# Kernel tuning notes

Hardware: AMD Instinct MI355X
Metric: run time of the kernel (lower is better)

## Reference

```python
import jax, jax.numpy as jnp
import numpy as np

N_NODES = 100000
N_EDGES = 1000000
D = 64
N_LAYERS = 3
N_GRAPHS = 64


def _sage_layer(x, src, dst, W_l, b_l, W_r, n_nodes):
    # PyG SAGEConv (aggr='mean'): out = lin_l(mean_{j in N(i)} x_j) + lin_r(x_i)
    msgs = x[src]  # [E, d] gather
    agg = jax.ops.segment_sum(msgs, dst, num_segments=n_nodes)  # [N, d]
    deg = jax.ops.segment_sum(jnp.ones((src.shape[0],), x.dtype), dst, num_segments=n_nodes)
    agg = agg / jnp.maximum(deg, 1.0)[:, None]
    return agg @ W_l + b_l + x @ W_r


def setup_inputs() -> dict:
    key = jax.random.key(0)
    k = jax.random.split(key, 6)
    scale = 1.0 / np.sqrt(D)
    x = jax.random.normal(k[0], (N_NODES, D), dtype=jnp.float32)
    edge_index = jax.random.randint(k[1], (2, N_EDGES), 0, N_NODES, dtype=jnp.int64)
    batch = jnp.sort(jax.random.randint(k[2], (N_NODES,), 0, N_GRAPHS, dtype=jnp.int64))
    Wl = jax.random.normal(k[3], (N_LAYERS, D, D), dtype=jnp.float32) * scale
    bl = jax.random.normal(k[4], (N_LAYERS, D), dtype=jnp.float32) * scale
    Wr = jax.random.normal(k[5], (N_LAYERS, D, D), dtype=jnp.float32) * scale
    return {"x": x, "edge_index": edge_index, "batch": batch,
            "Wl": Wl, "bl": bl, "Wr": Wr, "num_graphs": N_GRAPHS}


def reference(x, edge_index, batch, Wl, bl, Wr, num_graphs):
    src, dst = edge_index[0], edge_index[1]
    n_nodes = x.shape[0]
    for l in range(Wl.shape[0]):  # small fixed number of layers
        x = _sage_layer(x, src, dst, Wl[l], bl[l], Wr[l], n_nodes)
    # per-graph masked mean pooling == segment mean over batch ids
    sums = jax.ops.segment_sum(x, batch, num_segments=num_graphs)  # [G, d]
    counts = jax.ops.segment_sum(jnp.ones((n_nodes,), x.dtype), batch, num_segments=num_graphs)
    return sums / jnp.maximum(counts, 1.0)[:, None]
```

## Files before the change

### kernel.cpp

```cpp
#include <hip/hip_runtime.h>


#define DD 64
#define NBA 128
#define CAP 4096

typedef __attribute__((ext_vector_type(8))) short short8;
typedef __attribute__((ext_vector_type(4))) float f32x4;

__device__ inline short8 pack4(unsigned a, unsigned b, unsigned c, unsigned d) {
    union { uint4 u; short8 s; } un;
    un.u = make_uint4(a, b, c, d);
    return un.s;
}

__device__ inline short8 as_short8(uint4 u) {
    union { uint4 u4; short8 s; } un;
    un.u4 = u;
    return un.s;
}

__device__ inline unsigned rne_bf16(float v) {
    unsigned u = __float_as_uint(v);
    return (u + 0x7FFFu + ((u >> 16) & 1u)) >> 16;
}

__global__ __launch_bounds__(256) void bucket_count(
    const int* __restrict__ dst, int* __restrict__ cnt, int E, int NBUCK) {
    extern __shared__ int hist[];
    const int b = blockIdx.x;
    const int per = (E + NBA - 1) / NBA;
    const int lo = b * per, hi = min(lo + per, E);
    for (int k = threadIdx.x; k < NBUCK; k += 256) hist[k] = 0;
    __syncthreads();
    for (int e = lo + threadIdx.x; e < hi; e += 256)
        atomicAdd(&hist[dst[e] >> 8], 1);
    __syncthreads();
    for (int k = threadIdx.x; k < NBUCK; k += 256)
        cnt[b * NBUCK + k] = hist[k];
}

__global__ __launch_bounds__(256) void bucket_prescan(
    const int* __restrict__ cnt, int* __restrict__ base,
    int* __restrict__ tot, int NBUCK) {
    const int lane = threadIdx.x & 63;
    const int k = (int)((blockIdx.x * 256 + threadIdx.x) >> 6);
    if (k >= NBUCK) return;
    int v0 = cnt[(size_t)lane * NBUCK + k];
    int v1 = cnt[(size_t)(lane + 64) * NBUCK + k];
    int s0 = v0, s1 = v1;
#pragma unroll
    for (int o = 1; o < 64; o <<= 1) {
        const int u0 = __shfl_up(s0, o, 64);
        const int u1 = __shfl_up(s1, o, 64);
        if (lane >= o) { s0 += u0; s1 += u1; }
    }
    const int total0 = __shfl(s0, 63, 64);
    base[(size_t)lane * NBUCK + k] = s0 - v0;
    base[(size_t)(lane + 64) * NBUCK + k] = total0 + s1 - v1;
    if (lane == 63) tot[k] = total0 + s1;
}

__global__ __launch_bounds__(1024) void bucket_toff(
    const int* __restrict__ tot, int* __restrict__ boff,
    int* __restrict__ offs, int NBUCK, int E, int N) {
    __shared__ int s[1024];
    __shared__ int carry_s;
    const int t = threadIdx.x;
    if (t == 0) carry_s = 0;
    __syncthreads();
    for (int cs = 0; cs < NBUCK; cs += 1024) {
        const int i = cs + t;
        const int v = (i < NBUCK) ? tot[i] : 0;
        s[t] = v;
        __syncthreads();
        for (int o = 1; o < 1024; o <<= 1) {
            const int a = (t >= o) ? s[t - o] : 0;
            __syncthreads();
            s[t] += a;
            __syncthreads();
        }
        const int carry = carry_s;
        if (i < NBUCK) boff[i] = carry + s[t] - v;
        __syncthreads();
        if (t == 1023) carry_s = carry + s[1023];
        __syncthreads();
    }
    if (t == 0) { boff[NBUCK] = E; offs[N] = E; }
}

__global__ __launch_bounds__(256) void bucket_scatter(
    const int* __restrict__ src, const int* __restrict__ dst,
    const int* __restrict__ base, const int* __restrict__ boff,
    unsigned* __restrict__ ebuf, int E, int NBUCK) {
    extern __shared__ int pos[];
    const int b = blockIdx.x;
    const int per = (E + NBA - 1) / NBA;
    const int lo = b * per, hi = min(lo + per, E);
    for (int k = threadIdx.x; k < NBUCK; k += 256)
        pos[k] = base[b * NBUCK + k] + boff[k];
    __syncthreads();
    for (int e = lo + threadIdx.x; e < hi; e += 256) {
        const int d = dst[e];
        const int s = src[e];
        const int p = atomicAdd(&pos[d >> 8], 1);
        ebuf[p] = ((unsigned)(d & 255) << 24) | (unsigned)s;
    }
}

__global__ __launch_bounds__(256) void bucket_sort(
    const unsigned* __restrict__ ebuf, const int* __restrict__ boff,
    int* __restrict__ offs, int* __restrict__ adj, int N) {
    const int b  = blockIdx.x;
    const int lo = boff[b];
    const int sz = boff[b + 1] - lo;
    const int base = b << 8;
    const int t = threadIdx.x;

    __shared__ int hist[256];
    __shared__ int hcur[256];
    __shared__ unsigned sbuf[CAP];

    hist[t] = 0;
    __syncthreads();
    for (int i = t; i < sz; i += 256)
        atomicAdd(&hist[ebuf[lo + i] >> 24], 1);
    __syncthreads();
    int v = hist[t];
    hcur[t] = v;
    __syncthreads();
    for (int o = 1; o < 256; o <<= 1) {
        const int a = (t >= o) ? hcur[t - o] : 0;
        __syncthreads();
        hcur[t] += a;
        __syncthreads();
    }
    const int ex = hcur[t] - v;
    __syncthreads();
    hcur[t] = ex;
    if (base + t < N) offs[base + t] = lo + ex;
    __syncthreads();

    if (sz <= CAP) {
        for (int i = t; i < sz; i += 256) {
            const unsigned w = ebuf[lo + i];
            const int p = atomicAdd(&hcur[w >> 24], 1);
            sbuf[p] = w & 0x00FFFFFFu;
        }
        __syncthreads();
        for (int i = t; i < sz; i += 256) adj[lo + i] = (int)sbuf[i];
    } else {
        for (int i = t; i < sz; i += 256) {
            const unsigned w = ebuf[lo + i];
            const int p = atomicAdd(&hcur[w >> 24], 1);
            adj[lo + p] = (int)(w & 0x00FFFFFFu);
        }
    }
}

__global__ __launch_bounds__(256) void cast_bf16(
    const float* __restrict__ in, unsigned short* __restrict__ outb, long long n8) {
    const long long t = (long long)blockIdx.x * 256 + threadIdx.x;
    if (t >= n8) return;
    const float4 v0 = *reinterpret_cast<const float4*>(in + t * 8);
    const float4 v1 = *reinterpret_cast<const float4*>(in + t * 8 + 4);
    uint4 o;
    o.x = rne_bf16(v0.x) | (rne_bf16(v0.y) << 16);
    o.y = rne_bf16(v0.z) | (rne_bf16(v0.w) << 16);
    o.z = rne_bf16(v1.x) | (rne_bf16(v1.y) << 16);
    o.w = rne_bf16(v1.z) | (rne_bf16(v1.w) << 16);
    *reinterpret_cast<uint4*>(outb + t * 8) = o;
}

__global__ __launch_bounds__(256) void aggregate_bf16(
    const unsigned short* __restrict__ xb, unsigned short* __restrict__ aggb,
    const int* __restrict__ offs, const int* __restrict__ adj, int n) {
    const int t  = blockIdx.x * 256 + threadIdx.x;
    const int nd = t >> 3;
    const int c8 = (t & 7) * 8;
    if (nd >= n) return;

    const int s = offs[nd];
    const int e = offs[nd + 1];

    float a0[8], a1[8], a2[8], a3[8];
#pragma unroll
    for (int p = 0; p < 8; ++p) { a0[p] = 0.f; a1[p] = 0.f; a2[p] = 0.f; a3[p] = 0.f; }

#define ACC8(A, U)                                                             \
    do {                                                                       \
        A[0] += __uint_as_float((U).x << 16);                                  \
        A[1] += __uint_as_float((U).x & 0xFFFF0000u);                          \
        A[2] += __uint_as_float((U).y << 16);                                  \
        A[3] += __uint_as_float((U).y & 0xFFFF0000u);                          \
        A[4] += __uint_as_float((U).z << 16);                                  \
        A[5] += __uint_as_float((U).z & 0xFFFF0000u);                          \
        A[6] += __uint_as_float((U).w << 16);                                  \
        A[7] += __uint_as_float((U).w & 0xFFFF0000u);                          \
    } while (0)

    int j = s;
    for (; j + 8 <= e; j += 8) {
        const int i0 = adj[j],     i1 = adj[j + 1], i2 = adj[j + 2], i3 = adj[j + 3];
        const int i4 = adj[j + 4], i5 = adj[j + 5], i6 = adj[j + 6], i7 = adj[j + 7];
        const uint4 u0 = *reinterpret_cast<const uint4*>(xb + (size_t)i0 * DD + c8);
        const uint4 u1 = *reinterpret_cast<const uint4*>(xb + (size_t)i1 * DD + c8);
        const uint4 u2 = *reinterpret_cast<const uint4*>(xb + (size_t)i2 * DD + c8);
        const uint4 u3 = *reinterpret_cast<const uint4*>(xb + (size_t)i3 * DD + c8);
        const uint4 u4 = *reinterpret_cast<const uint4*>(xb + (size_t)i4 * DD + c8);
        const uint4 u5 = *reinterpret_cast<const uint4*>(xb + (size_t)i5 * DD + c8);
        const uint4 u6 = *reinterpret_cast<const uint4*>(xb + (size_t)i6 * DD + c8);
        const uint4 u7 = *reinterpret_cast<const uint4*>(xb + (size_t)i7 * DD + c8);
        ACC8(a0, u0); ACC8(a1, u1); ACC8(a2, u2); ACC8(a3, u3);
        ACC8(a0, u4); ACC8(a1, u5); ACC8(a2, u6); ACC8(a3, u7);
    }
    for (; j + 4 <= e; j += 4) {
        const int i0 = adj[j], i1 = adj[j + 1], i2 = adj[j + 2], i3 = adj[j + 3];
        const uint4 u0 = *reinterpret_cast<const uint4*>(xb + (size_t)i0 * DD + c8);
        const uint4 u1 = *reinterpret_cast<const uint4*>(xb + (size_t)i1 * DD + c8);
        const uint4 u2 = *reinterpret_cast<const uint4*>(xb + (size_t)i2 * DD + c8);
        const uint4 u3 = *reinterpret_cast<const uint4*>(xb + (size_t)i3 * DD + c8);
        ACC8(a0, u0); ACC8(a1, u1); ACC8(a2, u2); ACC8(a3, u3);
    }
    for (; j < e; ++j) {
        const uint4 u = *reinterpret_cast<const uint4*>(xb + (size_t)adj[j] * DD + c8);
        ACC8(a0, u);
    }
#undef ACC8

    const int deg = e - s;
    const float inv = (deg > 0) ? (1.0f / (float)deg) : 1.0f;
    float r[8];
#pragma unroll
    for (int p = 0; p < 8; ++p) r[p] = (a0[p] + a1[p] + a2[p] + a3[p]) * inv;
    uint4 o;
    o.x = rne_bf16(r[0]) | (rne_bf16(r[1]) << 16);
    o.y = rne_bf16(r[2]) | (rne_bf16(r[3]) << 16);
    o.z = rne_bf16(r[4]) | (rne_bf16(r[5]) << 16);
    o.w = rne_bf16(r[6]) | (rne_bf16(r[7]) << 16);
    *reinterpret_cast<uint4*>(aggb + (size_t)nd * DD + c8) = o;
}

__global__ void pack_B(const float* __restrict__ Wl, const float* __restrict__ Wr,
                       unsigned* __restrict__ Bp, int L) {
    int t = blockIdx.x * 256 + threadIdx.x;
    int wv = t >> 6, lane = t & 63;
    if (wv >= L * 16) return;
    int layer = wv >> 4;
    int fid = wv & 15;
    int ks = fid >> 2, nt = fid & 3;
    int j = nt * 16 + (lane & 15);
    int kb = ks * 32 + (lane >> 4) * 8;
    const float* wl = Wl + (size_t)layer * DD * DD;
    const float* wr = Wr + (size_t)layer * DD * DD;
    unsigned hi[8], lo[8];
#pragma unroll
    for (int s = 0; s < 8; ++s) {
        int k = kb + s;
        float v = (k < DD) ? wl[k * DD + j] : wr[(k - DD) * DD + j];
        unsigned u = __float_as_uint(v);
        unsigned h = u & 0xFFFF0000u;
        hi[s] = h;
        float lf = v - __uint_as_float(h);
        lo[s] = __float_as_uint(lf) & 0xFFFF0000u;
    }
    size_t base_hi = ((size_t)(layer * 2 + 0) * 16 + fid) * 64 + lane;
    size_t base_lo = ((size_t)(layer * 2 + 1) * 16 + fid) * 64 + lane;
#pragma unroll
    for (int p = 0; p < 4; ++p) {
        Bp[base_hi * 4 + p] = (hi[2 * p] >> 16) | hi[2 * p + 1];
        Bp[base_lo * 4 + p] = (lo[2 * p] >> 16) | lo[2 * p + 1];
    }
}

__global__ __launch_bounds__(256, 2) void mfma_gemm(
    const unsigned short* __restrict__ gb, const unsigned short* __restrict__ xb,
    unsigned short* __restrict__ outb, const unsigned* __restrict__ Bp,
    const float* __restrict__ bias, int n) {
    const int lane = threadIdx.x & 63;
    const int wv   = (int)((blockIdx.x * 256 + threadIdx.x) >> 6);
    const int nwv  = (int)((gridDim.x * 256) >> 6);

    short8 Bh[4][4], Bl[4][4];
#pragma unroll
    for (int ks = 0; ks < 4; ++ks)
#pragma unroll
        for (int nt = 0; nt < 4; ++nt) {
            int fid = ks * 4 + nt;
            const uint4 h = *reinterpret_cast<const uint4*>(Bp + ((size_t)fid * 64 + lane) * 4);
            const uint4 l = *reinterpret_cast<const uint4*>(Bp + ((size_t)(16 + fid) * 64 + lane) * 4);
            Bh[ks][nt] = pack4(h.x, h.y, h.z, h.w);
            Bl[ks][nt] = pack4(l.x, l.y, l.z, l.w);
        }

    float bv[4];
#pragma unroll
    for (int nt = 0; nt < 4; ++nt) bv[nt] = bias[nt * 16 + (lane & 15)];

    const int ntiles = (n + 15) >> 4;
    for (int tile = wv; tile < ntiles; tile += nwv) {
        const int row = tile * 16 + (lane & 15);
        const bool ok = row < n;
        const unsigned short* grow = gb + (size_t)row * DD + (lane >> 4) * 8;
        const unsigned short* xrow = xb + (size_t)row * DD + (lane >> 4) * 8;

        f32x4 acc[4];
#pragma unroll
        for (int nt = 0; nt < 4; ++nt) acc[nt] = (f32x4){bv[nt], bv[nt], bv[nt], bv[nt]};

#pragma unroll
        for (int ks = 0; ks < 4; ++ks) {
            const unsigned short* base = ((ks < 2) ? grow : xrow) + (ks & 1) * 32;
            const uint4 u = ok ? *reinterpret_cast<const uint4*>(base)
                               : make_uint4(0, 0, 0, 0);
            const short8 Ah = as_short8(u);
#pragma unroll
            for (int nt = 0; nt < 4; ++nt) {
                acc[nt] = __builtin_amdgcn_mfma_f32_16x16x32_bf16(Ah, Bh[ks][nt], acc[nt], 0, 0, 0);
                acc[nt] = __builtin_amdgcn_mfma_f32_16x16x32_bf16(Ah, Bl[ks][nt], acc[nt], 0, 0, 0);
            }
        }

        const int r0 = tile * 16 + (lane >> 4) * 4;
#pragma unroll
        for (int r = 0; r < 4; ++r) {
            const int rr = r0 + r;
            if (rr < n) {
#pragma unroll
                for (int nt = 0; nt < 4; ++nt) {
                    const size_t idx = (size_t)rr * DD + nt * 16 + (lane & 15);
                    outb[idx] = (unsigned short)rne_bf16(acc[nt][r]);
                }
            }
        }
    }
}

__global__ __launch_bounds__(256) void pool_partial2(
    const unsigned short* __restrict__ xa, const unsigned short* __restrict__ xb,
    const int* __restrict__ batch,
    float* __restrict__ sumsA, float* __restrict__ sumsB, int n) {
    const int lane = threadIdx.x & 63;
    const int wv   = (int)((blockIdx.x * blockDim.x + threadIdx.x) >> 6);
    const int nwv  = (int)((gridDim.x * blockDim.x) >> 6);
    const int chunk = (n + nwv - 1) / nwv;
    const int start = wv * chunk;
    if (start >= n) return;
    const int end = min(start + chunk, n);

    int g = batch[start];
    float accA = 0.f, accB = 0.f;
    for (int nd = start; nd < end; ++nd) {
        const int bg = batch[nd];
        if (bg != g) {
            atomicAdd(&sumsA[(size_t)g * DD + lane], accA);
            atomicAdd(&sumsB[(size_t)g * DD + lane], accB);
            accA = 0.f; accB = 0.f;
            g = bg;
        }
        accA += __uint_as_float((unsigned)xa[(size_t)nd * DD + lane] << 16);
        accB += __uint_as_float((unsigned)xb[(size_t)nd * DD + lane] << 16);
    }
    atomicAdd(&sumsA[(size_t)g * DD + lane], accA);
    atomicAdd(&sumsB[(size_t)g * DD + lane], accB);
}

__global__ void final_gemm(const float* __restrict__ sumsA, const float* __restrict__ sumsX,
                           const int* __restrict__ batch,
                           const float* __restrict__ Wl, const float* __restrict__ bl,
                           const float* __restrict__ Wr,
                           float* __restrict__ out, int n) {
    const int g = blockIdx.x;
    const int d = threadIdx.x;

    int lo = 0, hi = n;
    while (lo < hi) { int m = (lo + hi) >> 1; if (batch[m] < g) lo = m + 1; else hi = m; }
    const int st = lo;
    lo = 0; hi = n;
    while (lo < hi) { int m = (lo + hi) >> 1; if (batch[m] < g + 1) lo = m + 1; else hi = m; }
    const int c = lo - st;

    if (c == 0) {
        out[(size_t)g * DD + d] = 0.f;
        return;
    }
    const float inv = 1.0f / (float)c;

    __shared__ float sa[DD], sx[DD];
    sa[d] = sumsA[(size_t)g * DD + d] * inv;
    sx[d] = sumsX[(size_t)g * DD + d] * inv;
    __syncthreads();

    float acc = bl[d];
#pragma unroll 8
    for (int k = 0; k < DD; ++k) acc += sa[k] * Wl[k * DD + d];
#pragma unroll 8
    for (int k = 0; k < DD; ++k) acc += sx[k] * Wr[k * DD + d];
    out[(size_t)g * DD + d] = acc;
}

extern "C" void kernel_launch(void* const* d_in, const int* in_sizes, int n_in,
                              void* d_out, int out_size, void* d_ws, size_t ws_size,
                              hipStream_t stream) {
    const float* x     = (const float*)d_in[0];
    const int*   ei    = (const int*)d_in[1];
    const int*   batch = (const int*)d_in[2];
    const float* Wl    = (const float*)d_in[3];
    const float* bl    = (const float*)d_in[4];
    const float* Wr    = (const float*)d_in[5];

    const int N = in_sizes[0] / DD;
    const int E = in_sizes[1] / 2;
    const int L = in_sizes[3] / (DD * DD);
    const int G = out_size / DD;
    const int NBUCK = (N + 255) >> 8;

    const int* src = ei;
    const int* dst = ei + E;

    char* ws = (char*)d_ws;
    size_t off = 0;
    auto alloc = [&](size_t bytes) -> char* {
        char* p = ws + off;
        off += (bytes + 255) & ~(size_t)255;
        return p;
    };
    int*      offs   = (int*)alloc((size_t)(N + 1) * 4);
    int*      adj    = (int*)alloc((size_t)E * 4);
    int*      cnt    = (int*)alloc((size_t)NBA * NBUCK * 4);
    int*      basep  = (int*)alloc((size_t)NBA * NBUCK * 4);
    int*      boff   = (int*)alloc((size_t)(NBUCK + 1) * 4);
    int*      tot    = (int*)alloc((size_t)NBUCK * 4);
    unsigned* ebuf   = (unsigned*)alloc((size_t)E * 4);
    const size_t bfbytes = (size_t)N * DD * 2;
    unsigned short* aggb = (unsigned short*)alloc(bfbytes);
    unsigned* Bp     = (unsigned*)alloc((size_t)L * 2 * 16 * 64 * 4 * 4);
    float*    sumsA  = (float*)alloc((size_t)G * DD * 4);
    float*    sumsX  = (float*)alloc((size_t)G * DD * 4);
    unsigned short* bfIn = (unsigned short*)alloc(bfbytes);
    unsigned short* bf0  = (unsigned short*)alloc(bfbytes);

    const size_t ldsN = (size_t)NBUCK * 4;
    bucket_count<<<NBA, 256, ldsN, stream>>>(dst, cnt, E, NBUCK);
    bucket_prescan<<<(NBUCK * 64 + 255) / 256, 256, 0, stream>>>(cnt, basep, tot, NBUCK);
    bucket_toff<<<1, 1024, 0, stream>>>(tot, boff, offs, NBUCK, E, N);
    bucket_scatter<<<NBA, 256, ldsN, stream>>>(src, dst, basep, boff, ebuf, E, NBUCK);
    bucket_sort<<<NBUCK, 256, 0, stream>>>(ebuf, boff, offs, adj, N);

    pack_B<<<(L * 16 * 64 + 255) / 256, 256, 0, stream>>>(Wl, Wr, Bp, L);

    const long long n8 = (long long)N * DD / 8;
    cast_bf16<<<(int)((n8 + 255) / 256), 256, 0, stream>>>(x, bfIn, n8);

    const unsigned short* curb = bfIn;
    unsigned short* bfs[2] = {bf0, bfIn};
    const int aggB_blocks = (N * 8 + 255) / 256;
    for (int l = 0; l < L - 1; ++l) {
        aggregate_bf16<<<aggB_blocks, 256, 0, stream>>>(curb, aggb, offs, adj, N);
        mfma_gemm<<<1024, 256, 0, stream>>>(aggb, curb, bfs[l & 1],
                                            Bp + (size_t)l * 2 * 16 * 64 * 4,
                                            bl + (size_t)l * DD, N);
        curb = bfs[l & 1];
    }

    aggregate_bf16<<<aggB_blocks, 256, 0, stream>>>(curb, aggb, offs, adj, N);
    hipMemsetAsync(sumsA, 0, (size_t)G * DD * 4 * 2, stream);
    pool_partial2<<<2048, 256, 0, stream>>>(aggb, curb, batch, sumsA, sumsX, N);
    final_gemm<<<G, DD, 0, stream>>>(sumsA, sumsX, batch,
                                     Wl + (size_t)(L - 1) * DD * DD,
                                     bl + (size_t)(L - 1) * DD,
                                     Wr + (size_t)(L - 1) * DD * DD,
                                     (float*)d_out, N);
}
```

Baseline: 178.1 us.

## Fuse last-layer aggregation with pooling and merge small setup kernels

The final layer's mean aggregation now accumulates straight into per-graph sums through LDS atomics, so the bf16 agg buffer is no longer written and then re-read by the pooling pass. The bucket prescan and offset scan are merged into one kernel, where the last block to finish (found with an atomic done counter) performs the global scan. Weight packing and the input bf16 cast are merged into a single launch. Together these cut launch count and memory traffic, in exchange for atomic contention on pooled sums and float accumulation order that is no longer deterministic.

```diff
diff --git a/kernel.cpp b/kernel.cpp
--- a/kernel.cpp
+++ b/kernel.cpp
@@ -26,9 +26,11 @@
 }
 
 __global__ __launch_bounds__(256) void bucket_count(
-    const int* __restrict__ dst, int* __restrict__ cnt, int E, int NBUCK) {
+    const int* __restrict__ dst, int* __restrict__ cnt, int* __restrict__ done,
+    int E, int NBUCK) {
     extern __shared__ int hist[];
     const int b = blockIdx.x;
+    if (b == 0 && threadIdx.x == 0) *done = 0;
     const int per = (E + NBA - 1) / NBA;
     const int lo = b * per, hi = min(lo + per, E);
     for (int k = threadIdx.x; k < NBUCK; k += 256) hist[k] = 0;
@@ -40,50 +42,55 @@
         cnt[b * NBUCK + k] = hist[k];
 }
 
-__global__ __launch_bounds__(256) void bucket_prescan(
-    const int* __restrict__ cnt, int* __restrict__ base,
-    int* __restrict__ tot, int NBUCK) {
+__global__ __launch_bounds__(256) void bucket_prescan_toff(
+    const int* __restrict__ cnt, int* __restrict__ base, int* __restrict__ tot,
+    int* __restrict__ boff, int* __restrict__ offs, int* __restrict__ done,
+    int NBUCK, int E, int N) {
     const int lane = threadIdx.x & 63;
     const int k = (int)((blockIdx.x * 256 + threadIdx.x) >> 6);
-    if (k >= NBUCK) return;
-    int v0 = cnt[(size_t)lane * NBUCK + k];
-    int v1 = cnt[(size_t)(lane + 64) * NBUCK + k];
-    int s0 = v0, s1 = v1;
-#pragma unroll
-    for (int o = 1; o < 64; o <<= 1) {
-        const int u0 = __shfl_up(s0, o, 64);
-        const int u1 = __shfl_up(s1, o, 64);
-        if (lane >= o) { s0 += u0; s1 += u1; }
-    }
-    const int total0 = __shfl(s0, 63, 64);
-    base[(size_t)lane * NBUCK + k] = s0 - v0;
-    base[(size_t)(lane + 64) * NBUCK + k] = total0 + s1 - v1;
-    if (lane == 63) tot[k] = total0 + s1;
-}
-
-__global__ __launch_bounds__(1024) void bucket_toff(
-    const int* __restrict__ tot, int* __restrict__ boff,
-    int* __restrict__ offs, int NBUCK, int E, int N) {
-    __shared__ int s[1024];
+    if (k < NBUCK) {
+        int v0 = cnt[(size_t)lane * NBUCK + k];
+        int v1 = cnt[(size_t)(lane + 64) * NBUCK + k];
+        int s0 = v0, s1 = v1;
+#pragma unroll
+        for (int o = 1; o < 64; o <<= 1) {
+            const int u0 = __shfl_up(s0, o, 64);
+            const int u1 = __shfl_up(s1, o, 64);
+            if (lane >= o) { s0 += u0; s1 += u1; }
+        }
+        const int total0 = __shfl(s0, 63, 64);
+        base[(size_t)lane * NBUCK + k] = s0 - v0;
+        base[(size_t)(lane + 64) * NBUCK + k] = total0 + s1 - v1;
+        if (lane == 63) tot[k] = total0 + s1;
+    }
+    __threadfence();
+    __shared__ int lastflag;
+    if (threadIdx.x == 0)
+        lastflag = (atomicAdd(done, 1) == (int)gridDim.x - 1);
+    __syncthreads();
+    if (!lastflag) return;
+    __threadfence();
+
+    __shared__ int s[256];
     __shared__ int carry_s;
     const int t = threadIdx.x;
     if (t == 0) carry_s = 0;
     __syncthreads();
-    for (int cs = 0; cs < NBUCK; cs += 1024) {
+    for (int cs = 0; cs < NBUCK; cs += 256) {
         const int i = cs + t;
         const int v = (i < NBUCK) ? tot[i] : 0;
         s[t] = v;
         __syncthreads();
-        for (int o = 1; o < 1024; o <<= 1) {
+        for (int o = 1; o < 256; o <<= 1) {
             const int a = (t >= o) ? s[t - o] : 0;
             __syncthreads();
             s[t] += a;
             __syncthreads();
         }
-        const int carry = carry_s;
-        if (i < NBUCK) boff[i] = carry + s[t] - v;
+        const int c0 = carry_s;
+        if (i < NBUCK) boff[i] = c0 + s[t] - v;
         __syncthreads();
-        if (t == 1023) carry_s = carry + s[1023];
+        if (t == 255) carry_s = c0 + s[255];
         __syncthreads();
     }
     if (t == 0) { boff[NBUCK] = E; offs[N] = E; }
@@ -158,34 +165,53 @@
     }
 }
 
-__global__ __launch_bounds__(256) void cast_bf16(
-    const float* __restrict__ in, unsigned short* __restrict__ outb, long long n8) {
-    const long long t = (long long)blockIdx.x * 256 + threadIdx.x;
-    if (t >= n8) return;
-    const float4 v0 = *reinterpret_cast<const float4*>(in + t * 8);
-    const float4 v1 = *reinterpret_cast<const float4*>(in + t * 8 + 4);
-    uint4 o;
-    o.x = rne_bf16(v0.x) | (rne_bf16(v0.y) << 16);
-    o.y = rne_bf16(v0.z) | (rne_bf16(v0.w) << 16);
-    o.z = rne_bf16(v1.x) | (rne_bf16(v1.y) << 16);
-    o.w = rne_bf16(v1.z) | (rne_bf16(v1.w) << 16);
-    *reinterpret_cast<uint4*>(outb + t * 8) = o;
-}
-
-__global__ __launch_bounds__(256) void aggregate_bf16(
-    const unsigned short* __restrict__ xb, unsigned short* __restrict__ aggb,
-    const int* __restrict__ offs, const int* __restrict__ adj, int n) {
-    const int t  = blockIdx.x * 256 + threadIdx.x;
-    const int nd = t >> 3;
-    const int c8 = (t & 7) * 8;
-    if (nd >= n) return;
-
-    const int s = offs[nd];
-    const int e = offs[nd + 1];
-
-    float a0[8], a1[8], a2[8], a3[8];
-#pragma unroll
-    for (int p = 0; p < 8; ++p) { a0[p] = 0.f; a1[p] = 0.f; a2[p] = 0.f; a3[p] = 0.f; }
+__global__ __launch_bounds__(256) void prep(
+    const float* __restrict__ Wl, const float* __restrict__ Wr,
+    unsigned* __restrict__ Bp, int L,
+    const float* __restrict__ x, unsigned short* __restrict__ bfIn,
+    long long n8, int packBlocks) {
+    if ((int)blockIdx.x < packBlocks) {
+        int t = blockIdx.x * 256 + threadIdx.x;
+        int wv = t >> 6, lane = t & 63;
+        if (wv >= L * 16) return;
+        int layer = wv >> 4;
+        int fid = wv & 15;
+        int ks = fid >> 2, nt = fid & 3;
+        int j = nt * 16 + (lane & 15);
+        int kb = ks * 32 + (lane >> 4) * 8;
+        const float* wl = Wl + (size_t)layer * DD * DD;
+        const float* wr = Wr + (size_t)layer * DD * DD;
+        unsigned hi[8], lo[8];
+#pragma unroll
+        for (int s = 0; s < 8; ++s) {
+            int k = kb + s;
+            float v = (k < DD) ? wl[k * DD + j] : wr[(k - DD) * DD + j];
+            unsigned u = __float_as_uint(v);
+            unsigned h = u & 0xFFFF0000u;
+            hi[s] = h;
+            float lf = v - __uint_as_float(h);
+            lo[s] = __float_as_uint(lf) & 0xFFFF0000u;
+        }
+        size_t base_hi = ((size_t)(layer * 2 + 0) * 16 + fid) * 64 + lane;
+        size_t base_lo = ((size_t)(layer * 2 + 1) * 16 + fid) * 64 + lane;
+#pragma unroll
+        for (int p = 0; p < 4; ++p) {
+            Bp[base_hi * 4 + p] = (hi[2 * p] >> 16) | hi[2 * p + 1];
+            Bp[base_lo * 4 + p] = (lo[2 * p] >> 16) | lo[2 * p + 1];
+        }
+    } else {
+        const long long t = (long long)(blockIdx.x - packBlocks) * 256 + threadIdx.x;
+        if (t >= n8) return;
+        const float4 v0 = *reinterpret_cast<const float4*>(x + t * 8);
+        const float4 v1 = *reinterpret_cast<const float4*>(x + t * 8 + 4);
+        uint4 o;
+        o.x = rne_bf16(v0.x) | (rne_bf16(v0.y) << 16);
+        o.y = rne_bf16(v0.z) | (rne_bf16(v0.w) << 16);
+        o.z = rne_bf16(v1.x) | (rne_bf16(v1.y) << 16);
+        o.w = rne_bf16(v1.z) | (rne_bf16(v1.w) << 16);
+        *reinterpret_cast<uint4*>(bfIn + t * 8) = o;
+    }
+}
 
 #define ACC8(A, U)                                                             \
     do {                                                                       \
@@ -199,40 +225,53 @@
         A[7] += __uint_as_float((U).w & 0xFFFF0000u);                          \
     } while (0)
 
-    int j = s;
-    for (; j + 8 <= e; j += 8) {
-        const int i0 = adj[j],     i1 = adj[j + 1], i2 = adj[j + 2], i3 = adj[j + 3];
-        const int i4 = adj[j + 4], i5 = adj[j + 5], i6 = adj[j + 6], i7 = adj[j + 7];
-        const uint4 u0 = *reinterpret_cast<const uint4*>(xb + (size_t)i0 * DD + c8);
-        const uint4 u1 = *reinterpret_cast<const uint4*>(xb + (size_t)i1 * DD + c8);
-        const uint4 u2 = *reinterpret_cast<const uint4*>(xb + (size_t)i2 * DD + c8);
-        const uint4 u3 = *reinterpret_cast<const uint4*>(xb + (size_t)i3 * DD + c8);
-        const uint4 u4 = *reinterpret_cast<const uint4*>(xb + (size_t)i4 * DD + c8);
-        const uint4 u5 = *reinterpret_cast<const uint4*>(xb + (size_t)i5 * DD + c8);
-        const uint4 u6 = *reinterpret_cast<const uint4*>(xb + (size_t)i6 * DD + c8);
-        const uint4 u7 = *reinterpret_cast<const uint4*>(xb + (size_t)i7 * DD + c8);
-        ACC8(a0, u0); ACC8(a1, u1); ACC8(a2, u2); ACC8(a3, u3);
-        ACC8(a0, u4); ACC8(a1, u5); ACC8(a2, u6); ACC8(a3, u7);
-    }
-    for (; j + 4 <= e; j += 4) {
-        const int i0 = adj[j], i1 = adj[j + 1], i2 = adj[j + 2], i3 = adj[j + 3];
-        const uint4 u0 = *reinterpret_cast<const uint4*>(xb + (size_t)i0 * DD + c8);
-        const uint4 u1 = *reinterpret_cast<const uint4*>(xb + (size_t)i1 * DD + c8);
-        const uint4 u2 = *reinterpret_cast<const uint4*>(xb + (size_t)i2 * DD + c8);
-        const uint4 u3 = *reinterpret_cast<const uint4*>(xb + (size_t)i3 * DD + c8);
-        ACC8(a0, u0); ACC8(a1, u1); ACC8(a2, u2); ACC8(a3, u3);
-    }
-    for (; j < e; ++j) {
-        const uint4 u = *reinterpret_cast<const uint4*>(xb + (size_t)adj[j] * DD + c8);
-        ACC8(a0, u);
-    }
-#undef ACC8
-
-    const int deg = e - s;
-    const float inv = (deg > 0) ? (1.0f / (float)deg) : 1.0f;
+#define GATHER_BODY(XB, OFFS, ADJ, ND, C8, ROUT)                               \
+    float a0[8], a1[8], a2[8], a3[8];                                          \
+    _Pragma("unroll")                                                          \
+    for (int p = 0; p < 8; ++p) { a0[p]=0.f; a1[p]=0.f; a2[p]=0.f; a3[p]=0.f; }\
+    const int s_ = OFFS[ND];                                                   \
+    const int e_ = OFFS[ND + 1];                                               \
+    int j = s_;                                                                \
+    for (; j + 8 <= e_; j += 8) {                                              \
+        const int i0 = ADJ[j],     i1 = ADJ[j + 1], i2 = ADJ[j + 2], i3 = ADJ[j + 3]; \
+        const int i4 = ADJ[j + 4], i5 = ADJ[j + 5], i6 = ADJ[j + 6], i7 = ADJ[j + 7]; \
+        const uint4 u0 = *reinterpret_cast<const uint4*>(XB + (size_t)i0 * DD + C8); \
+        const uint4 u1 = *reinterpret_cast<const uint4*>(XB + (size_t)i1 * DD + C8); \
+        const uint4 u2 = *reinterpret_cast<const uint4*>(XB + (size_t)i2 * DD + C8); \
+        const uint4 u3 = *reinterpret_cast<const uint4*>(XB + (size_t)i3 * DD + C8); \
+        const uint4 u4 = *reinterpret_cast<const uint4*>(XB + (size_t)i4 * DD + C8); \
+        const uint4 u5 = *reinterpret_cast<const uint4*>(XB + (size_t)i5 * DD + C8); \
+        const uint4 u6 = *reinterpret_cast<const uint4*>(XB + (size_t)i6 * DD + C8); \
+        const uint4 u7 = *reinterpret_cast<const uint4*>(XB + (size_t)i7 * DD + C8); \
+        ACC8(a0, u0); ACC8(a1, u1); ACC8(a2, u2); ACC8(a3, u3);                \
+        ACC8(a0, u4); ACC8(a1, u5); ACC8(a2, u6); ACC8(a3, u7);                \
+    }                                                                          \
+    for (; j + 4 <= e_; j += 4) {                                              \
+        const int i0 = ADJ[j], i1 = ADJ[j + 1], i2 = ADJ[j + 2], i3 = ADJ[j + 3]; \
+        const uint4 u0 = *reinterpret_cast<const uint4*>(XB + (size_t)i0 * DD + C8); \
+        const uint4 u1 = *reinterpret_cast<const uint4*>(XB + (size_t)i1 * DD + C8); \
+        const uint4 u2 = *reinterpret_cast<const uint4*>(XB + (size_t)i2 * DD + C8); \
+        const uint4 u3 = *reinterpret_cast<const uint4*>(XB + (size_t)i3 * DD + C8); \
+        ACC8(a0, u0); ACC8(a1, u1); ACC8(a2, u2); ACC8(a3, u3);                \
+    }                                                                          \
+    for (; j < e_; ++j) {                                                      \
+        const uint4 u = *reinterpret_cast<const uint4*>(XB + (size_t)ADJ[j] * DD + C8); \
+        ACC8(a0, u);                                                           \
+    }                                                                          \
+    const int deg_ = e_ - s_;                                                  \
+    const float inv_ = (deg_ > 0) ? (1.0f / (float)deg_) : 1.0f;               \
+    _Pragma("unroll")                                                          \
+    for (int p = 0; p < 8; ++p) ROUT[p] = (a0[p] + a1[p] + a2[p] + a3[p]) * inv_;
+
+__global__ __launch_bounds__(256) void aggregate_bf16(
+    const unsigned short* __restrict__ xb, unsigned short* __restrict__ aggb,
+    const int* __restrict__ offs, const int* __restrict__ adj, int n) {
+    const int t  = blockIdx.x * 256 + threadIdx.x;
+    const int nd = t >> 3;
+    const int c8 = (t & 7) * 8;
+    if (nd >= n) return;
     float r[8];
-#pragma unroll
-    for (int p = 0; p < 8; ++p) r[p] = (a0[p] + a1[p] + a2[p] + a3[p]) * inv;
+    GATHER_BODY(xb, offs, adj, nd, c8, r)
     uint4 o;
     o.x = rne_bf16(r[0]) | (rne_bf16(r[1]) << 16);
     o.y = rne_bf16(r[2]) | (rne_bf16(r[3]) << 16);
@@ -241,35 +280,39 @@
     *reinterpret_cast<uint4*>(aggb + (size_t)nd * DD + c8) = o;
 }
 
-__global__ void pack_B(const float* __restrict__ Wl, const float* __restrict__ Wr,
-                       unsigned* __restrict__ Bp, int L) {
-    int t = blockIdx.x * 256 + threadIdx.x;
-    int wv = t >> 6, lane = t & 63;
-    if (wv >= L * 16) return;
-    int layer = wv >> 4;
-    int fid = wv & 15;
-    int ks = fid >> 2, nt = fid & 3;
-    int j = nt * 16 + (lane & 15);
-    int kb = ks * 32 + (lane >> 4) * 8;
-    const float* wl = Wl + (size_t)layer * DD * DD;
-    const float* wr = Wr + (size_t)layer * DD * DD;
-    unsigned hi[8], lo[8];
-#pragma unroll
-    for (int s = 0; s < 8; ++s) {
-        int k = kb + s;
-        float v = (k < DD) ? wl[k * DD + j] : wr[(k - DD) * DD + j];
-        unsigned u = __float_as_uint(v);
-        unsigned h = u & 0xFFFF0000u;
-        hi[s] = h;
-        float lf = v - __uint_as_float(h);
-        lo[s] = __float_as_uint(lf) & 0xFFFF0000u;
-    }
-    size_t base_hi = ((size_t)(layer * 2 + 0) * 16 + fid) * 64 + lane;
-    size_t base_lo = ((size_t)(layer * 2 + 1) * 16 + fid) * 64 + lane;
-#pragma unroll
-    for (int p = 0; p < 4; ++p) {
-        Bp[base_hi * 4 + p] = (hi[2 * p] >> 16) | hi[2 * p + 1];
-        Bp[base_lo * 4 + p] = (lo[2 * p] >> 16) | lo[2 * p + 1];
+__global__ __launch_bounds__(256) void aggregate_pool(
+    const unsigned short* __restrict__ xb,
+    const int* __restrict__ offs, const int* __restrict__ adj,
+    const int* __restrict__ batch, float* __restrict__ sumsA, int n, int G) {
+    const int t  = blockIdx.x * 256 + threadIdx.x;
+    const int nd = t >> 3;
+    const int c8 = (t & 7) * 8;
+
+    __shared__ float sl[2][DD];
+    if (threadIdx.x < 128) sl[threadIdx.x >> 6][threadIdx.x & 63] = 0.f;
+    __syncthreads();
+    const int b32 = (int)blockIdx.x * 32;
+    const int g0 = batch[(b32 < n - 1) ? b32 : (n - 1)];
+
+    if (nd < n) {
+        float r[8];
+        GATHER_BODY(xb, offs, adj, nd, c8, r)
+        const int slot = batch[nd] - g0;
+        if (slot < 2) {
+#pragma unroll
+            for (int p = 0; p < 8; ++p) atomicAdd(&sl[slot][c8 + p], r[p]);
+        } else {
+#pragma unroll
+            for (int p = 0; p < 8; ++p)
+                atomicAdd(&sumsA[(size_t)batch[nd] * DD + c8 + p], r[p]);
+        }
+    }
+    __syncthreads();
+    if (threadIdx.x < 128) {
+        const int s = threadIdx.x >> 6, d = threadIdx.x & 63;
+        const float v = sl[s][d];
+        if (v != 0.f && g0 + s < G)
+            atomicAdd(&sumsA[(size_t)(g0 + s) * DD + d], v);
     }
 }
 
@@ -336,10 +379,9 @@
     }
 }
 
-__global__ __launch_bounds__(256) void pool_partial2(
-    const unsigned short* __restrict__ xa, const unsigned short* __restrict__ xb,
-    const int* __restrict__ batch,
-    float* __restrict__ sumsA, float* __restrict__ sumsB, int n) {
+__global__ __launch_bounds__(256) void pool_x(
+    const unsigned short* __restrict__ xb, const int* __restrict__ batch,
+    float* __restrict__ sums, int n) {
     const int lane = threadIdx.x & 63;
     const int wv   = (int)((blockIdx.x * blockDim.x + threadIdx.x) >> 6);
     const int nwv  = (int)((gridDim.x * blockDim.x) >> 6);
@@ -349,20 +391,17 @@
     const int end = min(start + chunk, n);
 
     int g = batch[start];
-    float accA = 0.f, accB = 0.f;
+    float acc = 0.f;
     for (int nd = start; nd < end; ++nd) {
         const int bg = batch[nd];
         if (bg != g) {
-            atomicAdd(&sumsA[(size_t)g * DD + lane], accA);
-            atomicAdd(&sumsB[(size_t)g * DD + lane], accB);
-            accA = 0.f; accB = 0.f;
+            atomicAdd(&sums[(size_t)g * DD + lane], acc);
+            acc = 0.f;
             g = bg;
         }
-        accA += __uint_as_float((unsigned)xa[(size_t)nd * DD + lane] << 16);
-        accB += __uint_as_float((unsigned)xb[(size_t)nd * DD + lane] << 16);
-    }
-    atomicAdd(&sumsA[(size_t)g * DD + lane], accA);
-    atomicAdd(&sumsB[(size_t)g * DD + lane], accB);
+        acc += __uint_as_float((unsigned)xb[(size_t)nd * DD + lane] << 16);
+    }
+    atomicAdd(&sums[(size_t)g * DD + lane], acc);
 }
 
 __global__ void final_gemm(const float* __restrict__ sumsA, const float* __restrict__ sumsX,
@@ -431,6 +470,7 @@
     int*      basep  = (int*)alloc((size_t)NBA * NBUCK * 4);
     int*      boff   = (int*)alloc((size_t)(NBUCK + 1) * 4);
     int*      tot    = (int*)alloc((size_t)NBUCK * 4);
+    int*      done   = (int*)alloc(256);
     unsigned* ebuf   = (unsigned*)alloc((size_t)E * 4);
     const size_t bfbytes = (size_t)N * DD * 2;
     unsigned short* aggb = (unsigned short*)alloc(bfbytes);
@@ -441,16 +481,17 @@
     unsigned short* bf0  = (unsigned short*)alloc(bfbytes);
 
     const size_t ldsN = (size_t)NBUCK * 4;
-    bucket_count<<<NBA, 256, ldsN, stream>>>(dst, cnt, E, NBUCK);
-    bucket_prescan<<<(NBUCK * 64 + 255) / 256, 256, 0, stream>>>(cnt, basep, tot, NBUCK);
-    bucket_toff<<<1, 1024, 0, stream>>>(tot, boff, offs, NBUCK, E, N);
+    bucket_count<<<NBA, 256, ldsN, stream>>>(dst, cnt, done, E, NBUCK);
+    const int preBlocks = (NBUCK * 64 + 255) / 256;
+    bucket_prescan_toff<<<preBlocks, 256, 0, stream>>>(cnt, basep, tot, boff, offs,
+                                                       done, NBUCK, E, N);
     bucket_scatter<<<NBA, 256, ldsN, stream>>>(src, dst, basep, boff, ebuf, E, NBUCK);
     bucket_sort<<<NBUCK, 256, 0, stream>>>(ebuf, boff, offs, adj, N);
 
-    pack_B<<<(L * 16 * 64 + 255) / 256, 256, 0, stream>>>(Wl, Wr, Bp, L);
-
     const long long n8 = (long long)N * DD / 8;
-    cast_bf16<<<(int)((n8 + 255) / 256), 256, 0, stream>>>(x, bfIn, n8);
+    const int packBlocks = (L * 16 * 64 + 255) / 256;
+    prep<<<packBlocks + (int)((n8 + 255) / 256), 256, 0, stream>>>(
+        Wl, Wr, Bp, L, x, bfIn, n8, packBlocks);
 
     const unsigned short* curb = bfIn;
     unsigned short* bfs[2] = {bf0, bfIn};
@@ -463,9 +504,9 @@
         curb = bfs[l & 1];
     }
 
-    aggregate_bf16<<<aggB_blocks, 256, 0, stream>>>(curb, aggb, offs, adj, N);
-    hipMemsetAsync(sumsA, 0, (size_t)G * DD * 4 * 2, stream);
-    pool_partial2<<<2048, 256, 0, stream>>>(aggb, curb, batch, sumsA, sumsX, N);
+    (void)hipMemsetAsync(sumsA, 0, (size_t)G * DD * 4 * 2, stream);
+    aggregate_pool<<<aggB_blocks, 256, 0, stream>>>(curb, offs, adj, batch, sumsA, N, G);
+    pool_x<<<2048, 256, 0, stream>>>(curb, batch, sumsX, N);
     final_gemm<<<G, DD, 0, stream>>>(sumsA, sumsX, batch,
                                      Wl + (size_t)(L - 1) * DD * DD,
                                      bl + (size_t)(L - 1) * DD,
```

New measurement: 215.6 us. 1.21x slower.
